# Performance work log

Measured on AMD Instinct MI355X. Metric: run time of the kernel, lower is better.

## Reference

```python
import jax, jax.numpy as jnp
import numpy as np

K = 9                 # kernel_size (num_points)
CENTER = K // 2
EXTEND_SCOPE = 1.0
EPS = 1e-5
GROUPS = 4            # out_ch // 4


def _cumsum_from_center(o):
    # o: [N, K, D, W, H]; serial offset accumulation outward from center row,
    # vectorized as two cumsums (matches the torch for-loop recurrence).
    upper = jnp.cumsum(o[:, CENTER:], axis=1)                                   # rows c..K-1
    lower = jnp.flip(jnp.cumsum(jnp.flip(o[:, :CENTER + 1], axis=1), axis=1), axis=1)  # rows 0..c
    return jnp.concatenate([lower[:, :CENTER], upper], axis=1)


def _coordinate_map_3d(offset):
    # offset: [N, 3K, D, W, H] -> (z, y, x) coord maps, each [N, D, W, H*K]  (morph=0, if_offset=True)
    N, _, D, W, H = offset.shape
    dt = offset.dtype
    z_off, y_off, _x_off = jnp.split(offset, 3, axis=1)   # each [N, K, D, W, H]
    z_acc = _cumsum_from_center(z_off)
    y_acc = _cumsum_from_center(y_off)
    z_c = jnp.arange(D, dtype=dt)[None, None, :, None, None]
    y_c = jnp.arange(W, dtype=dt)[None, None, None, :, None]
    x_c = jnp.arange(H, dtype=dt)[None, None, None, None, :]
    x_g = (jnp.arange(K, dtype=dt) - CENTER)[None, :, None, None, None]  # linspace(-c, c, K)
    z_new = z_c + EXTEND_SCOPE * z_acc                 # [N, K, D, W, H]
    y_new = y_c + EXTEND_SCOPE * y_acc
    x_new = jnp.broadcast_to(x_c + x_g, z_new.shape)

    def pack(a):  # [N,K,D,W,H] -> [N,D,W,H*K] (permute(0,4,1,5,2,6,3) + reshape in torch)
        return jnp.transpose(a, (0, 2, 3, 4, 1)).reshape(N, D, W, H * K)

    return pack(z_new), pack(y_new), pack(x_new)


def _trilinear_interpolate(feat, z, y, x):
    # feat: [N, C, D, W, H]; z/y/x: [N, D, W, HK] -> [N, C, D, W, HK]
    N, C, D, W, H = feat.shape
    featp = jnp.transpose(feat, (0, 2, 3, 4, 1))  # [N, D, W, H, C]
    z0 = jnp.clip(jnp.floor(z).astype(jnp.int32), 0, D - 1)
    z1 = jnp.clip(jnp.floor(z).astype(jnp.int32) + 1, 0, D - 1)
    y0 = jnp.clip(jnp.floor(y).astype(jnp.int32), 0, W - 1)
    y1 = jnp.clip(jnp.floor(y).astype(jnp.int32) + 1, 0, W - 1)
    x0 = jnp.clip(jnp.floor(x).astype(jnp.int32), 0, H - 1)
    x1 = jnp.clip(jnp.floor(x).astype(jnp.int32) + 1, 0, H - 1)
    z0f, z1f = z0.astype(feat.dtype), z1.astype(feat.dtype)
    y0f, y1f = y0.astype(feat.dtype), y1.astype(feat.dtype)
    x0f, x1f = x0.astype(feat.dtype), x1.astype(feat.dtype)
    b = jnp.arange(N)[:, None, None, None]

    def g(zi, yi, xi):
        return featp[b, zi, yi, xi]  # gather -> [N, D, W, HK, C]

    out = (g(z0, y0, x0) * ((z1f - z) * (y1f - y) * (x1f - x))[..., None]
         + g(z0, y0, x1) * ((z1f - z) * (y1f - y) * (x - x0f))[..., None]
         + g(z0, y1, x0) * ((z1f - z) * (y - y0f) * (x1f - x))[..., None]
         + g(z0, y1, x1) * ((z1f - z) * (y - y0f) * (x - x0f))[..., None]
         + g(z1, y0, x0) * ((z - z0f) * (y1f - y) * (x1f - x))[..., None]
         + g(z1, y0, x1) * ((z - z0f) * (y1f - y) * (x - x0f))[..., None]
         + g(z1, y1, x0) * ((z - z0f) * (y - y0f) * (x1f - x))[..., None]
         + g(z1, y1, x1) * ((z - z0f) * (y - y0f) * (x - x0f))[..., None])
    return jnp.transpose(out, (0, 4, 1, 2, 3))  # [N, C, D, W, HK]


def _conv3d(x, w, b, stride, padding):
    out = jax.lax.conv_general_dilated(x, w, window_strides=stride, padding=padding,
                                       dimension_numbers=('NCDHW', 'OIDHW', 'NCDHW'))
    return out + b[None, :, None, None, None]


def _batchnorm(x, gamma, beta):
    mu = jnp.mean(x, axis=(0, 2, 3, 4), keepdims=True)
    var = jnp.var(x, axis=(0, 2, 3, 4), keepdims=True)
    xn = (x - mu) * jax.lax.rsqrt(var + EPS)
    return gamma[None, :, None, None, None] * xn + beta[None, :, None, None, None]


def _groupnorm(x, gamma, beta):
    N, C = x.shape[:2]
    xg = x.reshape(N, GROUPS, C // GROUPS, *x.shape[2:])
    mu = jnp.mean(xg, axis=(2, 3, 4, 5), keepdims=True)
    var = jnp.var(xg, axis=(2, 3, 4, 5), keepdims=True)
    xn = ((xg - mu) * jax.lax.rsqrt(var + EPS)).reshape(x.shape)
    return gamma[None, :, None, None, None] * xn + beta[None, :, None, None, None]


def setup_inputs() -> dict:
    key = jax.random.key(0)
    ks = jax.random.split(key, 5)
    N, Cin, Cout, D, W, H = 1, 8, 16, 64, 64, 64
    f = jax.random.normal(ks[0], (N, Cin, D, W, H), dtype=jnp.float32)
    off_w = jax.random.normal(ks[1], (3 * K, Cin, 3, 3, 3), dtype=jnp.float32) * 0.05
    off_b = jax.random.normal(ks[2], (3 * K,), dtype=jnp.float32) * 0.05
    bn_g = jnp.ones((3 * K,), jnp.float32)
    bn_b = jnp.zeros((3 * K,), jnp.float32)
    dcn_w = jax.random.normal(ks[3], (Cout, Cin, 1, 1, K), dtype=jnp.float32) * 0.1
    dcn_b = jax.random.normal(ks[4], (Cout,), dtype=jnp.float32) * 0.05
    gn_g = jnp.ones((Cout,), jnp.float32)
    gn_b = jnp.zeros((Cout,), jnp.float32)
    return {"f": f, "off_w": off_w, "off_b": off_b, "bn_g": bn_g, "bn_b": bn_b,
            "dcn_w": dcn_w, "dcn_b": dcn_b, "gn_g": gn_g, "gn_b": gn_b}


def reference(f, off_w, off_b, bn_g, bn_b, dcn_w, dcn_b, gn_g, gn_b):
    # offset branch: Conv3d(in, 3K, 3, pad 1) -> BN -> tanh
    offset = _conv3d(f, off_w, off_b, (1, 1, 1), [(1, 1), (1, 1), (1, 1)])
    offset = jnp.tanh(_batchnorm(offset, bn_g, bn_b))
    # deformable coordinate map (morph=0) + trilinear gather
    z, y, x = _coordinate_map_3d(offset)
    deformed = _trilinear_interpolate(f, z, y, x)        # [N, C, D, W, H*K]
    # fused conv along the extended axis: kernel (1,1,K), stride (1,1,K)
    out = _conv3d(deformed, dcn_w, dcn_b, (1, 1, K), [(0, 0), (0, 0), (0, 0)])
    return jax.nn.relu(_groupnorm(out, gn_g, gn_b))      # [N, out, D, W, H]
```

## Files before the change

### kernel.cpp

```cpp
#include <hip/hip_runtime.h>
#include <math.h>

#define VOX 262144

__device__ __forceinline__ int clampi(int v, int lo, int hi) {
    return v < lo ? lo : (v > hi ? hi : v);
}

__global__ void k_init(float* __restrict__ stats) {
    if (threadIdx.x < 64) stats[threadIdx.x] = 0.f;
}

__global__ void k_wt(const float* __restrict__ w, float* __restrict__ wT) {
    int i = blockIdx.x * 256 + threadIdx.x;
    if (i < 3888) {
        int c = i / 216, r = i % 216;
        int ci = r / 27, k = r % 27;
        wT[(k * 8 + ci) * 18 + c] = w[i];
    }
}

__global__ void k_transpose(const float* __restrict__ f, float* __restrict__ ft) {
    int idx = blockIdx.x * 256 + threadIdx.x;
    int x = idx & 63, y = (idx >> 6) & 63, z = (idx >> 12) & 63, ci = idx >> 18;
    ft[(((z * 64 + y) * 64 + x) << 3) + ci] = f[idx];
}

__global__ __launch_bounds__(256) void k_conv_off(
        const float* __restrict__ f, const float* __restrict__ wT,
        const float* __restrict__ b, float* __restrict__ offs,
        float* __restrict__ stats) {
    int idx = blockIdx.x * 256 + threadIdx.x;
    int h = idx & 63, wy = (idx >> 6) & 63, d = idx >> 12;

    int hc0 = h > 0 ? h - 1 : 0;
    int hc2 = h < 63 ? h + 1 : 63;
    float mh0 = h > 0 ? 1.f : 0.f;
    float mh2 = h < 63 ? 1.f : 0.f;

    float acc[18];
#pragma unroll
    for (int c = 0; c < 18; c++) acc[c] = b[c];

#pragma unroll
    for (int kd = 0; kd < 3; kd++) {
        int dd = d + kd - 1;
#pragma unroll
        for (int kw = 0; kw < 3; kw++) {
            int ww = wy + kw - 1;
            bool ok = ((unsigned)dd < 64u) & ((unsigned)ww < 64u);
            const float* fp = f + (dd * 64 + ww) * 64;
            const float* wrow = wT + ((kd * 3 + kw) * 3) * 8 * 18;
            if (ok) {
#pragma unroll
                for (int ci = 0; ci < 8; ci++) {
                    float v0 = fp[ci * VOX + hc0] * mh0;
                    float v1 = fp[ci * VOX + h];
                    float v2 = fp[ci * VOX + hc2] * mh2;
                    const float* wp = wrow + ci * 18;
#pragma unroll
                    for (int c = 0; c < 18; c++) {
                        float a = acc[c];
                        a = fmaf(v0, wp[c], a);
                        a = fmaf(v1, wp[144 + c], a);
                        a = fmaf(v2, wp[288 + c], a);
                        acc[c] = a;
                    }
                }
            }
        }
    }

#pragma unroll
    for (int c = 0; c < 18; c++) offs[c * VOX + idx] = acc[c];

    __shared__ float ls[36];
    if (threadIdx.x < 36) ls[threadIdx.x] = 0.f;
    __syncthreads();
#pragma unroll
    for (int c = 0; c < 18; c++) {
        float s = acc[c], q = acc[c] * acc[c];
#pragma unroll
        for (int o = 32; o > 0; o >>= 1) {
            s += __shfl_xor(s, o);
            q += __shfl_xor(q, o);
        }
        if ((threadIdx.x & 63) == 0) {
            atomicAdd(&ls[c], s);
            atomicAdd(&ls[18 + c], q);
        }
    }
    __syncthreads();
    if (threadIdx.x < 36) atomicAdd(&stats[threadIdx.x], ls[threadIdx.x]);
}

__global__ __launch_bounds__(256) void k_main(
        const float* __restrict__ ft, const float* __restrict__ offs,
        const float* __restrict__ stats, const float* __restrict__ bn_g,
        const float* __restrict__ bn_b, const float* __restrict__ dw,
        const float* __restrict__ db, float* __restrict__ out,
        float* __restrict__ gstats) {
    int idx = blockIdx.x * 256 + threadIdx.x;
    int h = idx & 63, wy = (idx >> 6) & 63, d = idx >> 12;
    const float inv = 1.f / (float)VOX;

    float zo[9], yo[9];
#pragma unroll
    for (int c = 0; c < 18; c++) {
        float m = stats[c] * inv;
        float var = stats[18 + c] * inv - m * m;
        float rs = rsqrtf(var + 1e-5f);
        float t = tanhf(bn_g[c] * ((offs[c * VOX + idx] - m) * rs) + bn_b[c]);
        if (c < 9) zo[c] = t; else yo[c - 9] = t;
    }

    float za[9], ya[9];
    za[4] = zo[4]; ya[4] = yo[4];
#pragma unroll
    for (int k = 5; k < 9; k++) { za[k] = za[k - 1] + zo[k]; ya[k] = ya[k - 1] + yo[k]; }
#pragma unroll
    for (int k = 3; k >= 0; k--) { za[k] = za[k + 1] + zo[k]; ya[k] = ya[k + 1] + yo[k]; }

    float acc[16];
#pragma unroll
    for (int co = 0; co < 16; co++) acc[co] = db[co];

#pragma unroll
    for (int k = 0; k < 9; k++) {
        int xi = h + k - 4;
        if (xi >= 0 && xi <= 62) {
            float z = (float)d + za[k];
            float y = (float)wy + ya[k];
            float fz = floorf(z), fy = floorf(y);
            int iz = (int)fz, iy = (int)fy;
            int z0 = clampi(iz, 0, 63), z1 = clampi(iz + 1, 0, 63);
            int y0 = clampi(iy, 0, 63), y1 = clampi(iy + 1, 0, 63);
            float wz0 = (float)z1 - z, wz1 = z - (float)z0;
            float wy0 = (float)y1 - y, wy1 = y - (float)y0;
            float w00 = wz0 * wy0, w01 = wz0 * wy1, w10 = wz1 * wy0, w11 = wz1 * wy1;

            const float4* p00 = (const float4*)(ft + (((z0 * 64 + y0) * 64 + xi) << 3));
            const float4* p01 = (const float4*)(ft + (((z0 * 64 + y1) * 64 + xi) << 3));
            const float4* p10 = (const float4*)(ft + (((z1 * 64 + y0) * 64 + xi) << 3));
            const float4* p11 = (const float4*)(ft + (((z1 * 64 + y1) * 64 + xi) << 3));
            float4 a00 = p00[0], b00 = p00[1];
            float4 a01 = p01[0], b01 = p01[1];
            float4 a10 = p10[0], b10 = p10[1];
            float4 a11 = p11[0], b11 = p11[1];

            float v[8];
            v[0] = w00 * a00.x + w01 * a01.x + w10 * a10.x + w11 * a11.x;
            v[1] = w00 * a00.y + w01 * a01.y + w10 * a10.y + w11 * a11.y;
            v[2] = w00 * a00.z + w01 * a01.z + w10 * a10.z + w11 * a11.z;
            v[3] = w00 * a00.w + w01 * a01.w + w10 * a10.w + w11 * a11.w;
            v[4] = w00 * b00.x + w01 * b01.x + w10 * b10.x + w11 * b11.x;
            v[5] = w00 * b00.y + w01 * b01.y + w10 * b10.y + w11 * b11.y;
            v[6] = w00 * b00.z + w01 * b01.z + w10 * b10.z + w11 * b11.z;
            v[7] = w00 * b00.w + w01 * b01.w + w10 * b10.w + w11 * b11.w;

#pragma unroll
            for (int ci = 0; ci < 8; ci++) {
#pragma unroll
                for (int co = 0; co < 16; co++)
                    acc[co] = fmaf(v[ci], dw[(co * 8 + ci) * 9 + k], acc[co]);
            }
        }
    }

#pragma unroll
    for (int co = 0; co < 16; co++) out[co * VOX + idx] = acc[co];

    __shared__ float ls[8];
    if (threadIdx.x < 8) ls[threadIdx.x] = 0.f;
    __syncthreads();
#pragma unroll
    for (int g = 0; g < 4; g++) {
        float s = acc[4 * g] + acc[4 * g + 1] + acc[4 * g + 2] + acc[4 * g + 3];
        float q = acc[4 * g] * acc[4 * g] + acc[4 * g + 1] * acc[4 * g + 1]
                + acc[4 * g + 2] * acc[4 * g + 2] + acc[4 * g + 3] * acc[4 * g + 3];
#pragma unroll
        for (int o = 32; o > 0; o >>= 1) {
            s += __shfl_xor(s, o);
            q += __shfl_xor(q, o);
        }
        if ((threadIdx.x & 63) == 0) {
            atomicAdd(&ls[g], s);
            atomicAdd(&ls[4 + g], q);
        }
    }
    __syncthreads();
    if (threadIdx.x < 8) atomicAdd(&gstats[threadIdx.x], ls[threadIdx.x]);
}

__global__ void k_gn(const float* __restrict__ gstats, const float* __restrict__ gn_g,
                     const float* __restrict__ gn_b, float* __restrict__ out) {
    int idx = blockIdx.x * 256 + threadIdx.x;
    int c = idx >> 18;
    int g = c >> 2;
    const float invn = 1.f / (4.f * (float)VOX);
    float m = gstats[g] * invn;
    float var = gstats[4 + g] * invn - m * m;
    float rs = rsqrtf(var + 1e-5f);
    float v = (out[idx] - m) * rs * gn_g[c] + gn_b[c];
    out[idx] = v > 0.f ? v : 0.f;
}

extern "C" void kernel_launch(void* const* d_in, const int* in_sizes, int n_in,
                              void* d_out, int out_size, void* d_ws, size_t ws_size,
                              hipStream_t stream) {
    const float* f    = (const float*)d_in[0];
    const float* offw = (const float*)d_in[1];
    const float* offb = (const float*)d_in[2];
    const float* bng  = (const float*)d_in[3];
    const float* bnb  = (const float*)d_in[4];
    const float* dcnw = (const float*)d_in[5];
    const float* dcnb = (const float*)d_in[6];
    const float* gng  = (const float*)d_in[7];
    const float* gnb  = (const float*)d_in[8];
    float* out = (float*)d_out;

    float* ws    = (float*)d_ws;
    float* ft    = ws;
    float* offs  = ws + 8 * VOX;
    float* stats = offs + 18 * VOX;
    float* gstats = stats + 36;
    float* wT = out;

    hipLaunchKernelGGL(k_init, dim3(1), dim3(64), 0, stream, stats);
    hipLaunchKernelGGL(k_wt, dim3(16), dim3(256), 0, stream, offw, wT);
    hipLaunchKernelGGL(k_transpose, dim3((8 * VOX) / 256), dim3(256), 0, stream, f, ft);
    hipLaunchKernelGGL(k_conv_off, dim3(VOX / 256), dim3(256), 0, stream,
                       f, wT, offb, offs, stats);
    hipLaunchKernelGGL(k_main, dim3(VOX / 256), dim3(256), 0, stream,
                       ft, offs, stats, bng, bnb, dcnw, dcnb, out, gstats);
    hipLaunchKernelGGL(k_gn, dim3((16 * VOX) / 256), dim3(256), 0, stream,
                       gstats, gng, gnb, out);
}
```

Measured before the change: 195.3 us.

## Split conv and gather work across two thread groups per voxel, fuse setup kernels

The three small setup kernels (stats zeroing, weight transpose, input transpose) become one launch. In the offset conv and the main gather kernel, each voxel is now handled by two threads that split the 9 kernel taps (5 and 4), with partial accumulators combined through shared memory. This doubles the thread count, for more parallelism and latency hiding. The offset conv takes its neighbouring-x inputs via wavefront shuffles instead of extra global loads, and tanhf is replaced with an exp-based fast tanh, which is slightly less accurate.

```diff
diff --git a/kernel.cpp b/kernel.cpp
--- a/kernel.cpp
+++ b/kernel.cpp
@@ -7,56 +7,69 @@
     return v < lo ? lo : (v > hi ? hi : v);
 }
 
-__global__ void k_init(float* __restrict__ stats) {
-    if (threadIdx.x < 64) stats[threadIdx.x] = 0.f;
-}
-
-__global__ void k_wt(const float* __restrict__ w, float* __restrict__ wT) {
-    int i = blockIdx.x * 256 + threadIdx.x;
-    if (i < 3888) {
-        int c = i / 216, r = i % 216;
-        int ci = r / 27, k = r % 27;
-        wT[(k * 8 + ci) * 18 + c] = w[i];
-    }
-}
-
-__global__ void k_transpose(const float* __restrict__ f, float* __restrict__ ft) {
-    int idx = blockIdx.x * 256 + threadIdx.x;
-    int x = idx & 63, y = (idx >> 6) & 63, z = (idx >> 12) & 63, ci = idx >> 18;
-    ft[(((z * 64 + y) * 64 + x) << 3) + ci] = f[idx];
+__device__ __forceinline__ float fast_tanh(float x) {
+    float e = __expf(2.f * x);
+    return 1.f - 2.f / (e + 1.f);
+}
+
+__global__ void k_setup(const float* __restrict__ f, float* __restrict__ ft,
+                        float* __restrict__ stats, const float* __restrict__ w,
+                        float* __restrict__ wT) {
+    int bid = blockIdx.x;
+    if (bid < 8192) {
+        int idx = bid * 256 + threadIdx.x;
+        int x = idx & 63, y = (idx >> 6) & 63, z = (idx >> 12) & 63, ci = idx >> 18;
+        ft[(((z * 64 + y) * 64 + x) << 3) + ci] = f[idx];
+    } else if (bid == 8192) {
+        if (threadIdx.x < 64) stats[threadIdx.x] = 0.f;
+    } else {
+        int i = (bid - 8193) * 256 + threadIdx.x;
+        if (i < 3888) {
+            int c = i / 216, r = i % 216;
+            int ci = r / 27, k = r % 27;
+            wT[(k * 8 + ci) * 18 + c] = w[i];
+        }
+    }
 }
 
 __global__ __launch_bounds__(256) void k_conv_off(
         const float* __restrict__ f, const float* __restrict__ wT,
         const float* __restrict__ b, float* __restrict__ offs,
         float* __restrict__ stats) {
-    int idx = blockIdx.x * 256 + threadIdx.x;
-    int h = idx & 63, wy = (idx >> 6) & 63, d = idx >> 12;
-
-    int hc0 = h > 0 ? h - 1 : 0;
-    int hc2 = h < 63 ? h + 1 : 63;
+    __shared__ float part[128 * 19];
+    __shared__ float ls[36];
+    if (threadIdx.x < 36) ls[threadIdx.x] = 0.f;
+
+    int lv = threadIdx.x & 127;
+    int grp = threadIdx.x >> 7;
+    int lane = threadIdx.x & 63;
+    int vox = blockIdx.x * 128 + lv;
+    int h = vox & 63, wy = (vox >> 6) & 63, d = vox >> 12;
+
     float mh0 = h > 0 ? 1.f : 0.f;
     float mh2 = h < 63 ? 1.f : 0.f;
+    int sl0 = lane > 0 ? lane - 1 : 0;
+    int sl2 = lane < 63 ? lane + 1 : 63;
 
     float acc[18];
 #pragma unroll
-    for (int c = 0; c < 18; c++) acc[c] = b[c];
-
-#pragma unroll
-    for (int kd = 0; kd < 3; kd++) {
-        int dd = d + kd - 1;
-#pragma unroll
-        for (int kw = 0; kw < 3; kw++) {
+    for (int c = 0; c < 18; c++) acc[c] = grp ? 0.f : b[c];
+
+#pragma unroll
+    for (int p = 0; p < 9; p++) {
+        if ((grp == 0) == (p < 5)) {
+            int kd = p / 3, kw = p % 3;
+            int dd = d + kd - 1;
             int ww = wy + kw - 1;
             bool ok = ((unsigned)dd < 64u) & ((unsigned)ww < 64u);
-            const float* fp = f + (dd * 64 + ww) * 64;
-            const float* wrow = wT + ((kd * 3 + kw) * 3) * 8 * 18;
             if (ok) {
+                const float* fp = f + (dd * 64 + ww) * 64 + h;
+                const float* wrow = wT + (p * 3) * 8 * 18;
 #pragma unroll
                 for (int ci = 0; ci < 8; ci++) {
-                    float v0 = fp[ci * VOX + hc0] * mh0;
-                    float v1 = fp[ci * VOX + h];
-                    float v2 = fp[ci * VOX + hc2] * mh2;
+                    float v1 = fp[ci * VOX];
+                    float v0 = __shfl(v1, sl0) * mh0;
+                    float v2 = __shfl(v1, sl2) * mh2;
                     const float* wp = wrow + ci * 18;
 #pragma unroll
                     for (int c = 0; c < 18; c++) {
@@ -71,23 +84,29 @@
         }
     }
 
-#pragma unroll
-    for (int c = 0; c < 18; c++) offs[c * VOX + idx] = acc[c];
-
-    __shared__ float ls[36];
-    if (threadIdx.x < 36) ls[threadIdx.x] = 0.f;
-    __syncthreads();
-#pragma unroll
-    for (int c = 0; c < 18; c++) {
-        float s = acc[c], q = acc[c] * acc[c];
-#pragma unroll
-        for (int o = 32; o > 0; o >>= 1) {
-            s += __shfl_xor(s, o);
-            q += __shfl_xor(q, o);
-        }
-        if ((threadIdx.x & 63) == 0) {
-            atomicAdd(&ls[c], s);
-            atomicAdd(&ls[18 + c], q);
+    if (grp == 1) {
+#pragma unroll
+        for (int c = 0; c < 18; c++) part[lv * 19 + c] = acc[c];
+    }
+    __syncthreads();
+
+    if (grp == 0) {
+#pragma unroll
+        for (int c = 0; c < 18; c++) acc[c] += part[lv * 19 + c];
+#pragma unroll
+        for (int c = 0; c < 18; c++) offs[c * VOX + vox] = acc[c];
+#pragma unroll
+        for (int c = 0; c < 18; c++) {
+            float s = acc[c], q = acc[c] * acc[c];
+#pragma unroll
+            for (int o = 32; o > 0; o >>= 1) {
+                s += __shfl_xor(s, o);
+                q += __shfl_xor(q, o);
+            }
+            if (lane == 0) {
+                atomicAdd(&ls[c], s);
+                atomicAdd(&ls[18 + c], q);
+            }
         }
     }
     __syncthreads();
@@ -100,8 +119,15 @@
         const float* __restrict__ bn_b, const float* __restrict__ dw,
         const float* __restrict__ db, float* __restrict__ out,
         float* __restrict__ gstats) {
-    int idx = blockIdx.x * 256 + threadIdx.x;
-    int h = idx & 63, wy = (idx >> 6) & 63, d = idx >> 12;
+    __shared__ float part[128 * 17];
+    __shared__ float ls[8];
+    if (threadIdx.x < 8) ls[threadIdx.x] = 0.f;
+
+    int lv = threadIdx.x & 127;
+    int grp = threadIdx.x >> 7;
+    int lane = threadIdx.x & 63;
+    int vox = blockIdx.x * 128 + lv;
+    int h = vox & 63, wy = (vox >> 6) & 63, d = vox >> 12;
     const float inv = 1.f / (float)VOX;
 
     float zo[9], yo[9];
@@ -110,7 +136,7 @@
         float m = stats[c] * inv;
         float var = stats[18 + c] * inv - m * m;
         float rs = rsqrtf(var + 1e-5f);
-        float t = tanhf(bn_g[c] * ((offs[c * VOX + idx] - m) * rs) + bn_b[c]);
+        float t = fast_tanh(bn_g[c] * ((offs[c * VOX + vox] - m) * rs) + bn_b[c]);
         if (c < 9) zo[c] = t; else yo[c - 9] = t;
     }
 
@@ -123,69 +149,77 @@
 
     float acc[16];
 #pragma unroll
-    for (int co = 0; co < 16; co++) acc[co] = db[co];
+    for (int co = 0; co < 16; co++) acc[co] = grp ? 0.f : db[co];
 
 #pragma unroll
     for (int k = 0; k < 9; k++) {
-        int xi = h + k - 4;
-        if (xi >= 0 && xi <= 62) {
-            float z = (float)d + za[k];
-            float y = (float)wy + ya[k];
-            float fz = floorf(z), fy = floorf(y);
-            int iz = (int)fz, iy = (int)fy;
-            int z0 = clampi(iz, 0, 63), z1 = clampi(iz + 1, 0, 63);
-            int y0 = clampi(iy, 0, 63), y1 = clampi(iy + 1, 0, 63);
-            float wz0 = (float)z1 - z, wz1 = z - (float)z0;
-            float wy0 = (float)y1 - y, wy1 = y - (float)y0;
-            float w00 = wz0 * wy0, w01 = wz0 * wy1, w10 = wz1 * wy0, w11 = wz1 * wy1;
-
-            const float4* p00 = (const float4*)(ft + (((z0 * 64 + y0) * 64 + xi) << 3));
-            const float4* p01 = (const float4*)(ft + (((z0 * 64 + y1) * 64 + xi) << 3));
-            const float4* p10 = (const float4*)(ft + (((z1 * 64 + y0) * 64 + xi) << 3));
-            const float4* p11 = (const float4*)(ft + (((z1 * 64 + y1) * 64 + xi) << 3));
-            float4 a00 = p00[0], b00 = p00[1];
-            float4 a01 = p01[0], b01 = p01[1];
-            float4 a10 = p10[0], b10 = p10[1];
-            float4 a11 = p11[0], b11 = p11[1];
-
-            float v[8];
-            v[0] = w00 * a00.x + w01 * a01.x + w10 * a10.x + w11 * a11.x;
-            v[1] = w00 * a00.y + w01 * a01.y + w10 * a10.y + w11 * a11.y;
-            v[2] = w00 * a00.z + w01 * a01.z + w10 * a10.z + w11 * a11.z;
-            v[3] = w00 * a00.w + w01 * a01.w + w10 * a10.w + w11 * a11.w;
-            v[4] = w00 * b00.x + w01 * b01.x + w10 * b10.x + w11 * b11.x;
-            v[5] = w00 * b00.y + w01 * b01.y + w10 * b10.y + w11 * b11.y;
-            v[6] = w00 * b00.z + w01 * b01.z + w10 * b10.z + w11 * b11.z;
-            v[7] = w00 * b00.w + w01 * b01.w + w10 * b10.w + w11 * b11.w;
-
-#pragma unroll
-            for (int ci = 0; ci < 8; ci++) {
-#pragma unroll
-                for (int co = 0; co < 16; co++)
-                    acc[co] = fmaf(v[ci], dw[(co * 8 + ci) * 9 + k], acc[co]);
-            }
-        }
-    }
-
-#pragma unroll
-    for (int co = 0; co < 16; co++) out[co * VOX + idx] = acc[co];
-
-    __shared__ float ls[8];
-    if (threadIdx.x < 8) ls[threadIdx.x] = 0.f;
-    __syncthreads();
-#pragma unroll
-    for (int g = 0; g < 4; g++) {
-        float s = acc[4 * g] + acc[4 * g + 1] + acc[4 * g + 2] + acc[4 * g + 3];
-        float q = acc[4 * g] * acc[4 * g] + acc[4 * g + 1] * acc[4 * g + 1]
-                + acc[4 * g + 2] * acc[4 * g + 2] + acc[4 * g + 3] * acc[4 * g + 3];
-#pragma unroll
-        for (int o = 32; o > 0; o >>= 1) {
-            s += __shfl_xor(s, o);
-            q += __shfl_xor(q, o);
-        }
-        if ((threadIdx.x & 63) == 0) {
-            atomicAdd(&ls[g], s);
-            atomicAdd(&ls[4 + g], q);
+        if ((grp == 0) == (k < 5)) {
+            int xi = h + k - 4;
+            if (xi >= 0 && xi <= 62) {
+                float z = (float)d + za[k];
+                float y = (float)wy + ya[k];
+                int iz = (int)floorf(z), iy = (int)floorf(y);
+                int z0 = clampi(iz, 0, 63), z1 = clampi(iz + 1, 0, 63);
+                int y0 = clampi(iy, 0, 63), y1 = clampi(iy + 1, 0, 63);
+                float wz0 = (float)z1 - z, wz1 = z - (float)z0;
+                float wy0 = (float)y1 - y, wy1 = y - (float)y0;
+                float w00 = wz0 * wy0, w01 = wz0 * wy1, w10 = wz1 * wy0, w11 = wz1 * wy1;
+
+                const float4* p00 = (const float4*)(ft + (((z0 * 64 + y0) * 64 + xi) << 3));
+                const float4* p01 = (const float4*)(ft + (((z0 * 64 + y1) * 64 + xi) << 3));
+                const float4* p10 = (const float4*)(ft + (((z1 * 64 + y0) * 64 + xi) << 3));
+                const float4* p11 = (const float4*)(ft + (((z1 * 64 + y1) * 64 + xi) << 3));
+                float4 a00 = p00[0], b00 = p00[1];
+                float4 a01 = p01[0], b01 = p01[1];
+                float4 a10 = p10[0], b10 = p10[1];
+                float4 a11 = p11[0], b11 = p11[1];
+
+                float v[8];
+                v[0] = w00 * a00.x + w01 * a01.x + w10 * a10.x + w11 * a11.x;
+                v[1] = w00 * a00.y + w01 * a01.y + w10 * a10.y + w11 * a11.y;
+                v[2] = w00 * a00.z + w01 * a01.z + w10 * a10.z + w11 * a11.z;
+                v[3] = w00 * a00.w + w01 * a01.w + w10 * a10.w + w11 * a11.w;
+                v[4] = w00 * b00.x + w01 * b01.x + w10 * b10.x + w11 * b11.x;
+                v[5] = w00 * b00.y + w01 * b01.y + w10 * b10.y + w11 * b11.y;
+                v[6] = w00 * b00.z + w01 * b01.z + w10 * b10.z + w11 * b11.z;
+                v[7] = w00 * b00.w + w01 * b01.w + w10 * b10.w + w11 * b11.w;
+
+#pragma unroll
+                for (int ci = 0; ci < 8; ci++) {
+#pragma unroll
+                    for (int co = 0; co < 16; co++)
+                        acc[co] = fmaf(v[ci], dw[(co * 8 + ci) * 9 + k], acc[co]);
+                }
+            }
+        }
+    }
+
+    if (grp == 1) {
+#pragma unroll
+        for (int co = 0; co < 16; co++) part[lv * 17 + co] = acc[co];
+    }
+    __syncthreads();
+
+    if (grp == 0) {
+#pragma unroll
+        for (int co = 0; co < 16; co++) acc[co] += part[lv * 17 + co];
+#pragma unroll
+        for (int co = 0; co < 16; co++) out[co * VOX + vox] = acc[co];
+
+#pragma unroll
+        for (int g = 0; g < 4; g++) {
+            float s = acc[4 * g] + acc[4 * g + 1] + acc[4 * g + 2] + acc[4 * g + 3];
+            float q = acc[4 * g] * acc[4 * g] + acc[4 * g + 1] * acc[4 * g + 1]
+                    + acc[4 * g + 2] * acc[4 * g + 2] + acc[4 * g + 3] * acc[4 * g + 3];
+#pragma unroll
+            for (int o = 32; o > 0; o >>= 1) {
+                s += __shfl_xor(s, o);
+                q += __shfl_xor(q, o);
+            }
+            if (lane == 0) {
+                atomicAdd(&ls[g], s);
+                atomicAdd(&ls[4 + g], q);
+            }
         }
     }
     __syncthreads();
@@ -219,19 +253,17 @@
     const float* gnb  = (const float*)d_in[8];
     float* out = (float*)d_out;
 
-    float* ws    = (float*)d_ws;
-    float* ft    = ws;
-    float* offs  = ws + 8 * VOX;
-    float* stats = offs + 18 * VOX;
+    float* ws     = (float*)d_ws;
+    float* ft     = ws;
+    float* offs   = ws + 8 * VOX;
+    float* stats  = offs + 18 * VOX;
     float* gstats = stats + 36;
     float* wT = out;
 
-    hipLaunchKernelGGL(k_init, dim3(1), dim3(64), 0, stream, stats);
-    hipLaunchKernelGGL(k_wt, dim3(16), dim3(256), 0, stream, offw, wT);
-    hipLaunchKernelGGL(k_transpose, dim3((8 * VOX) / 256), dim3(256), 0, stream, f, ft);
-    hipLaunchKernelGGL(k_conv_off, dim3(VOX / 256), dim3(256), 0, stream,
+    hipLaunchKernelGGL(k_setup, dim3(8209), dim3(256), 0, stream, f, ft, stats, offw, wT);
+    hipLaunchKernelGGL(k_conv_off, dim3(2048), dim3(256), 0, stream,
                        f, wT, offb, offs, stats);
-    hipLaunchKernelGGL(k_main, dim3(VOX / 256), dim3(256), 0, stream,
+    hipLaunchKernelGGL(k_main, dim3(2048), dim3(256), 0, stream,
                        ft, offs, stats, bng, bnb, dcnw, dcnb, out, gstats);
     hipLaunchKernelGGL(k_gn, dim3((16 * VOX) / 256), dim3(256), 0, stream,
                        gstats, gng, gnb, out);
```

Result: slower. 217.2 us (+11.2%).
